# Kernel tuning notes

Hardware: AMD Instinct MI355X
Metric: run time of the kernel (lower is better)

## Reference

```python
import jax, jax.numpy as jnp
import numpy as np

LN_EPS = 1e-5


def _pos_embed_2d(w, h, c, dtype=jnp.float32):
    # matches build_2d_sincos_position_embedding: meshgrid indexing='xy' -> (h, w) grids
    grid_w = jnp.arange(w, dtype=jnp.float32)
    grid_h = jnp.arange(h, dtype=jnp.float32)
    gw, gh = jnp.meshgrid(grid_w, grid_h, indexing='xy')  # each (h, w)
    pos_dim = c // 4
    omega = 1.0 / (10000.0 ** (jnp.arange(pos_dim, dtype=jnp.float32) / pos_dim))
    out_w = gw.reshape(-1, 1) * omega[None]  # (h*w, pos_dim)
    out_h = gh.reshape(-1, 1) * omega[None]
    pe = jnp.concatenate([jnp.sin(out_w), jnp.cos(out_w), jnp.sin(out_h), jnp.cos(out_h)], axis=1)
    return pe.astype(dtype)  # (h*w, c)


def setup_inputs() -> dict:
    key = jax.random.key(0)
    k1, k2 = jax.random.split(key)
    N, C, H, W = 16, 256, 40, 40
    x = jax.random.normal(k1, (N, C, H, W), dtype=jnp.float32)
    ln_w = jnp.ones((C,), dtype=jnp.float32)
    ln_b = jnp.zeros((C,), dtype=jnp.float32)
    qkv_w = jax.random.normal(k2, (3 * C, C), dtype=jnp.float32) * 0.02  # 1x1 conv weight
    qkv_b = jnp.zeros((3 * C,), dtype=jnp.float32)
    gamma = jnp.ones((1,), dtype=jnp.float32)
    return {"x": x, "ln_w": ln_w, "ln_b": ln_b, "qkv_w": qkv_w, "qkv_b": qkv_b, "gamma": gamma}


def reference(x, ln_w, ln_b, qkv_w, qkv_b, gamma):
    N, C, H, W = x.shape
    scale = C ** (-0.5)
    identity = x

    # LayerNorm over channels (computed in NHWC like the torch permute dance)
    xh = jnp.transpose(x, (0, 2, 3, 1))  # (N, H, W, C)
    mu = jnp.mean(xh, axis=-1, keepdims=True)
    var = jnp.mean(jnp.square(xh - mu), axis=-1, keepdims=True)
    xn = (xh - mu) * jax.lax.rsqrt(var + LN_EPS) * ln_w + ln_b

    # 1x1 conv == per-pixel linear
    qkv = jnp.einsum('nhwc,oc->nhwo', xn, qkv_w) + qkv_b  # (N, H, W, 3C)
    qkv = qkv.reshape(N, H * W, 3 * C)
    q, k, v = jnp.split(qkv, 3, axis=-1)  # each (N, HW, C)

    pe = _pos_embed_2d(W, H, C, x.dtype)  # (HW, C)
    q = q + pe
    k = k + pe

    attn = jax.nn.softmax(jnp.einsum('nqc,nkc->nqk', q, k) * scale, axis=-1)
    out = jnp.einsum('nqk,nkc->nqc', attn, v)  # (N, HW, C)
    out = jnp.transpose(out, (0, 2, 1)).reshape(N, C, H, W)
    return identity + gamma[0] * out
```

## Files before the change

kernel.cpp:

```cpp
#include <hip/hip_runtime.h>
#include <hip/hip_bf16.h>

typedef float f32x4 __attribute__((ext_vector_type(4)));
typedef float f32x16 __attribute__((ext_vector_type(16)));
typedef __bf16 v8bf __attribute__((ext_vector_type(8)));
typedef unsigned short ushortx4 __attribute__((ext_vector_type(4)));
typedef unsigned short ushortx8 __attribute__((ext_vector_type(8)));
typedef unsigned int uint4v __attribute__((ext_vector_type(4)));

#define NIMG 16
#define CCH  256
#define HWP  1600

#define QSCALE 0.09016844f
#define DEFER_THR 2.885390f

__device__ __forceinline__ unsigned short f2bf(float f) {
  unsigned int u = __builtin_bit_cast(unsigned int, f);
  u = (u + 0x7FFFu + ((u >> 16) & 1u)) >> 16;
  return (unsigned short)u;
}

__device__ __forceinline__ f32x4 mfma16(v8bf a, v8bf b, f32x4 c) {
  return __builtin_amdgcn_mfma_f32_16x16x32_bf16(a, b, c, 0, 0, 0);
}

__device__ __forceinline__ unsigned cvtpk(float a, float b) {
  unsigned r;
  asm("v_cvt_pk_bf16_f32 %0, %1, %2" : "=v"(r) : "v"(a), "v"(b));
  return r;
}
__device__ __forceinline__ float exp2v(float x) {
  float r;
  asm("v_exp_f32 %0, %1" : "=v"(r) : "v"(x));
  return r;
}
__device__ __forceinline__ float sin2pi(float rev) {
  float r;
  asm("v_fract_f32 %0, %1\n\tv_sin_f32 %0, %0" : "=v"(r) : "v"(rev));
  return r;
}
#define PSWAP(a, b) asm("v_permlane32_swap_b32 %0, %1" : "+v"(a), "+v"(b))

__global__ void prep_kernel(const float* __restrict__ qkv_w,
                            float* __restrict__ pe,
                            unsigned short* __restrict__ w_frag) {
  int tid = blockIdx.x * blockDim.x + threadIdx.x;
  int nthr = gridDim.x * blockDim.x;
  for (int i = tid; i < 768 * 256; i += nthr) {
    int o = i >> 8, c = i & 255;
    int tile = o >> 4, lr = o & 15;
    int ks = c >> 5, lg = (c >> 3) & 3, e = c & 7;
    w_frag[(((size_t)tile * 8 + ks) * 64 + lg * 16 + lr) * 8 + e] = f2bf(qkv_w[i]);
  }
  const float oc = 0.20762051f;
  const float inv2pi = 0.15915494f;
  for (int i = tid; i < HWP * 256; i += nthr) {
    int p = i >> 8, c = i & 255;
    int j = p % 40, ii = p / 40;
    int tt = c & 63;
    float omega = exp2v(-(float)tt * oc) * inv2pi;
    float coord = (c < 128) ? (float)j : (float)ii;
    float rev = coord * omega;
    if (c & 64) rev += 0.25f;
    pe[i] = sin2pi(rev);
  }
}

__global__ __launch_bounds__(512, 4) void ln_qkv_kernel(
    const float* __restrict__ x, const float* __restrict__ ln_w, const float* __restrict__ ln_b,
    const unsigned short* __restrict__ w_frag, const float* __restrict__ qkv_b,
    const float* __restrict__ pe,
    unsigned short* __restrict__ q_arr, unsigned short* __restrict__ k_arr,
    unsigned short* __restrict__ v_arr) {
  __shared__ unsigned short bufraw[18432];
  __shared__ float red_s[8][64], red_q[8][64];
  __shared__ float mu_s[64], rs_s[64];

  int t = threadIdx.x;
  int n = blockIdx.x / 25, pt = blockIdx.x % 25;
  int pix0 = pt * 64;
  int p = t & 63, g = t >> 6;
  const float* xb = x + (size_t)n * CCH * HWP + pix0;

  {
    float sum = 0.f, sq = 0.f;
#pragma unroll
    for (int i = 0; i < 32; ++i) {
      float v = xb[(size_t)(g * 32 + i) * HWP + p];
      sum += v; sq += v * v;
    }
    red_s[g][p] = sum; red_q[g][p] = sq;
  }
  __syncthreads();
  if (t < 64) {
    float s = 0.f, q2 = 0.f;
#pragma unroll
    for (int gg = 0; gg < 8; ++gg) { s += red_s[gg][t]; q2 += red_q[gg][t]; }
    float mu = s * (1.f / 256.f);
    float var = q2 * (1.f / 256.f) - mu * mu;
    mu_s[t] = mu;
    rs_s[t] = rsqrtf(var + 1e-5f);
  }
  __syncthreads();
  {
    float mu = mu_s[p], rs = rs_s[p];
    int p7 = p & 7;
#pragma unroll
    for (int i4 = 0; i4 < 8; ++i4) {
      int c0 = g * 32 + i4 * 4;
      f32x4 lw = *(const f32x4*)&ln_w[c0];
      f32x4 lb = *(const f32x4*)&ln_b[c0];
      ushortx4 pk;
#pragma unroll
      for (int r = 0; r < 4; ++r) {
        float v = xb[(size_t)(c0 + r) * HWP + p];
        pk[r] = f2bf((v - mu) * rs * lw[r] + lb[r]);
      }
      int unit = (c0 >> 3) ^ p7;
      *(ushortx4*)&bufraw[p * 256 + unit * 8 + (i4 & 1) * 4] = pk;
    }
  }
  __syncthreads();

  int w = t >> 6, l = t & 63, lr = l & 15, lg = l >> 4;
  int lr7 = lr & 7;
  f32x4 acc[6][4];
#pragma unroll
  for (int nf = 0; nf < 6; ++nf)
#pragma unroll
    for (int mi = 0; mi < 4; ++mi) acc[nf][mi] = (f32x4){0.f, 0.f, 0.f, 0.f};

#pragma unroll
  for (int ks = 0; ks < 8; ++ks) {
    v8bf bF[4];
#pragma unroll
    for (int mi = 0; mi < 4; ++mi)
      bF[mi] = *(const v8bf*)&bufraw[(mi * 16 + lr) * 256 + (((ks * 4 + lg) ^ lr7) * 8)];
#pragma unroll
    for (int nf = 0; nf < 6; ++nf) {
      int tile = w + nf * 8;
      v8bf wf = *(const v8bf*)&w_frag[(((size_t)tile * 8 + ks) * 64 + l) * 8];
#pragma unroll
      for (int mi = 0; mi < 4; ++mi) acc[nf][mi] = mfma16(wf, bF[mi], acc[nf][mi]);
    }
  }
  __syncthreads();

  int lgh = lg >> 1, lgl = lg & 1;

#pragma unroll
  for (int nf = 4; nf < 6; ++nf) {
    int tile = w + nf * 8;
    f32x4 bi = *(const f32x4*)&qkv_b[tile * 16 + lg * 4];
    int chb = (nf - 4) * 16 + lg * 4;
#pragma unroll
    for (int mi = 0; mi < 4; ++mi) {
      int pixl = mi * 16 + lr;
      f32x4 vv = acc[nf][mi] + bi;
#pragma unroll
      for (int r = 0; r < 4; ++r)
        bufraw[(w * 32 + chb + r) * 72 + pixl] = f2bf(vv[r]);
    }
  }

#pragma unroll
  for (int nf = 0; nf < 2; ++nf) {
    int tile = w + nf * 8;
    f32x4 bi = *(const f32x4*)&qkv_b[tile * 16 + lg * 4];
#pragma unroll
    for (int mi = 0; mi < 4; ++mi) {
      int pix = pix0 + mi * 16 + lr;
      f32x4 pev = *(const f32x4*)&pe[(size_t)pix * 256 + tile * 16 + lg * 4];
      f32x4 vv = (acc[nf][mi] + bi + pev) * QSCALE;
      ushortx4 pk = {f2bf(vv[0]), f2bf(vv[1]), f2bf(vv[2]), f2bf(vv[3])};
      int qt = pix >> 5, l31 = pix & 31;
      size_t ad = ((((size_t)n * 50 + qt) * 16 + tile) * 2 + lgh) * 256 + l31 * 8 + lgl * 4;
      *(ushortx4*)&q_arr[ad] = pk;
    }
  }
#pragma unroll
  for (int nf = 2; nf < 4; ++nf) {
    int tile = w + nf * 8;
    int dt = tile - 16;
    f32x4 bi = *(const f32x4*)&qkv_b[tile * 16 + lg * 4];
#pragma unroll
    for (int mi = 0; mi < 4; ++mi) {
      int pix = pix0 + mi * 16 + lr;
      f32x4 pev = *(const f32x4*)&pe[(size_t)pix * 256 + dt * 16 + lg * 4];
      f32x4 vv = acc[nf][mi] + bi + pev;
      ushortx4 pk = {f2bf(vv[0]), f2bf(vv[1]), f2bf(vv[2]), f2bf(vv[3])};
      size_t ad = (((size_t)n * 16 + dt) * 1600 + pix) * 16 + lgh * 8 + lgl * 4;
      *(ushortx4*)&k_arr[ad] = pk;
    }
  }

#pragma unroll
  for (int c = 0; c < 4; ++c) {
    int ch = l & 31;
    int pg = (l >> 5) + c * 2;
    ushortx8 vv = *(const ushortx8*)&bufraw[(w * 32 + ch) * 72 + pg * 8];
    int kvsl = pg >> 1, hi2 = pg & 1;
    int d = (ch & 15) + w * 16 + (ch >> 4) * 128;
    size_t di = (((size_t)n * 100 + pt * 4 + kvsl) * 2 + hi2) * 256 + d;
    *(ushortx8*)&v_arr[di * 8] = vv;
  }
}

__global__ __launch_bounds__(128, 2) void attn_kernel(
    const unsigned short* __restrict__ q_arr, const unsigned short* __restrict__ k_arr,
    const unsigned short* __restrict__ v_arr, const float* __restrict__ x,
    const float* __restrict__ gamma, float* __restrict__ out) {
  __shared__ float sx[4][2][4][64][4];

  int t = threadIdx.x;
  int wv = t >> 6, l = t & 63;
  int l31 = l & 31, hi = l >> 5;
  int dto = wv * 8;
  int dto32 = wv * 4;
  int slot = blockIdx.x & 7, j = blockIdx.x >> 3;
  int n = slot + 8 * (j / 50);
  int qt = j % 50;
  int q0 = qt * 32;

  v8bf qf[8];
  {
    const unsigned short* qp = q_arr + (((size_t)n * 50 + qt) * 32 + hi) * 256 + l31 * 8;
#pragma unroll
    for (int i = 0; i < 8; ++i)
      qf[i] = *(const v8bf*)(qp + (dto + i) * 512);
  }

  f32x16 acc[4];
#pragma unroll
  for (int dd = 0; dd < 4; ++dd)
#pragma unroll
    for (int r = 0; r < 16; ++r) acc[dd][r] = 0.f;

  float m_run = -1e30f, l_run = 0.f;

  const unsigned short* kbase = k_arr + (size_t)n * (16 * 1600 * 16) +
                                (size_t)dto * 25600 + hi * 8;
  const unsigned short* vbase = v_arr + (size_t)n * (100 * 2 * 256 * 8) +
                                hi * 2048 + l31 * 8 + dto32 * 256;

  v8bf kc[8];
#pragma unroll
  for (int i = 0; i < 8; ++i)
    kc[i] = *(const v8bf*)(kbase + (size_t)i * 25600 + l31 * 16);

  f32x16 sA, sB;
#pragma unroll
  for (int r = 0; r < 16; ++r) sA[r] = 0.f;
#pragma unroll
  for (int i = 0; i < 8; ++i)
    sA = __builtin_amdgcn_mfma_f32_32x32x16_bf16(kc[i], qf[i], sA, 0, 0, 0);

#pragma unroll
  for (int r4 = 0; r4 < 4; ++r4) {
    f32x4 vv = {sA[r4 * 4 + 0], sA[r4 * 4 + 1], sA[r4 * 4 + 2], sA[r4 * 4 + 3]};
    *(f32x4*)&sx[0][wv][r4][l][0] = vv;
  }
#pragma unroll
  for (int i = 0; i < 8; ++i)
    kc[i] = *(const v8bf*)(kbase + (size_t)i * 25600 + (32 + l31) * 16);

  v8bf vf0[4], vf1[4];
#pragma unroll
  for (int i = 0; i < 4; ++i) vf0[i] = *(const v8bf*)(vbase + i * 256);
#pragma unroll
  for (int i = 0; i < 4; ++i) vf1[i] = *(const v8bf*)(vbase + 4096 + i * 256);

  auto body = [&](int kt, f32x16& scur, f32x16& snxt, bool nexttile) {
    asm volatile("s_waitcnt lgkmcnt(0)" ::: "memory");
    __builtin_amdgcn_s_barrier();
    int br = kt & 3;
    float p[16];
#pragma unroll
    for (int r4 = 0; r4 < 4; ++r4) {
      f32x4 oth = *(const f32x4*)&sx[br][wv ^ 1][r4][l][0];
#pragma unroll
      for (int rr = 0; rr < 4; ++rr)
        p[r4 * 4 + rr] = scur[r4 * 4 + rr] + oth[rr];
    }
    if (nexttile) {
#pragma unroll
      for (int r = 0; r < 16; ++r) snxt[r] = 0.f;
#pragma unroll
      for (int i = 0; i < 4; ++i)
        snxt = __builtin_amdgcn_mfma_f32_32x32x16_bf16(kc[i], qf[i], snxt, 0, 0, 0);
    }
    float t0 = fmaxf(p[0], p[1]), t1 = fmaxf(p[2], p[3]);
    float t2 = fmaxf(p[4], p[5]), t3 = fmaxf(p[6], p[7]);
    float t4 = fmaxf(p[8], p[9]), t5 = fmaxf(p[10], p[11]);
    float t6 = fmaxf(p[12], p[13]), t7 = fmaxf(p[14], p[15]);
    float mx = fmaxf(fmaxf(fmaxf(t0, t1), fmaxf(t2, t3)),
                     fmaxf(fmaxf(t4, t5), fmaxf(t6, t7)));
    mx = fmaxf(mx, __shfl_xor(mx, 32));
    if (!__all(mx <= m_run + DEFER_THR)) {
      float mnew = fmaxf(m_run, mx);
      float alpha = exp2v(m_run - mnew);
      l_run *= alpha;
#pragma unroll
      for (int dd = 0; dd < 4; ++dd)
#pragma unroll
        for (int r = 0; r < 16; ++r) acc[dd][r] *= alpha;
      m_run = mnew;
    }
    if (nexttile) {
#pragma unroll
      for (int i = 4; i < 8; ++i)
        snxt = __builtin_amdgcn_mfma_f32_32x32x16_bf16(kc[i], qf[i], snxt, 0, 0, 0);
    }
#pragma unroll
    for (int r = 0; r < 16; ++r) p[r] = exp2v(p[r] - m_run);
    float sSum = ((p[0] + p[1]) + (p[2] + p[3])) + ((p[4] + p[5]) + (p[6] + p[7])) +
                 (((p[8] + p[9]) + (p[10] + p[11])) + ((p[12] + p[13]) + (p[14] + p[15])));
    sSum += __shfl_xor(sSum, 32);
    l_run += sSum;

    unsigned x0 = cvtpk(p[0], p[1]), x1 = cvtpk(p[2], p[3]);
    unsigned y0 = cvtpk(p[4], p[5]), y1 = cvtpk(p[6], p[7]);
    PSWAP(x0, y0); PSWAP(x1, y1);
    uint4v u0 = {x0, x1, y0, y1};
    v8bf pf0 = __builtin_bit_cast(v8bf, u0);
    unsigned z0 = cvtpk(p[8], p[9]), z1 = cvtpk(p[10], p[11]);
    unsigned w0 = cvtpk(p[12], p[13]), w1 = cvtpk(p[14], p[15]);
    PSWAP(z0, w0); PSWAP(z1, w1);
    uint4v u1 = {z0, z1, w0, w1};
    v8bf pf1 = __builtin_bit_cast(v8bf, u1);

#pragma unroll
    for (int dd = 0; dd < 4; ++dd) {
      acc[dd] = __builtin_amdgcn_mfma_f32_32x32x16_bf16(vf0[dd], pf0, acc[dd], 0, 0, 0);
      acc[dd] = __builtin_amdgcn_mfma_f32_32x32x16_bf16(vf1[dd], pf1, acc[dd], 0, 0, 0);
    }

    if (nexttile) {
      int bw = (kt + 1) & 3;
#pragma unroll
      for (int r4 = 0; r4 < 4; ++r4) {
        f32x4 vv = {snxt[r4 * 4 + 0], snxt[r4 * 4 + 1], snxt[r4 * 4 + 2], snxt[r4 * 4 + 3]};
        *(f32x4*)&sx[bw][wv][r4][l][0] = vv;
      }
      int kt2 = (kt + 2 < 50) ? kt + 2 : 0;
#pragma unroll
      for (int i = 0; i < 8; ++i)
        kc[i] = *(const v8bf*)(kbase + (size_t)i * 25600 + (kt2 * 32 + l31) * 16);
      const unsigned short* vp = vbase + (size_t)(kt + 1) * 8192;
#pragma unroll
      for (int i = 0; i < 4; ++i) vf0[i] = *(const v8bf*)(vp + i * 256);
#pragma unroll
      for (int i = 0; i < 4; ++i) vf1[i] = *(const v8bf*)(vp + 4096 + i * 256);
    }
  };

  for (int kt = 0; kt < 48; kt += 2) {
    body(kt, sA, sB, true);
    body(kt + 1, sB, sA, true);
  }
  body(48, sA, sB, true);
  body(49, sB, sA, false);

  float inv = 1.f / l_run;
  float gm = gamma[0];
#pragma unroll
  for (int dd = 0; dd < 4; ++dd) {
#pragma unroll
    for (int r = 0; r < 16; ++r) {
      int d = (dto32 + dd) * 32 + (r & 3) + 8 * (r >> 2) + 4 * hi;
      size_t base = ((size_t)n * 256 + d) * HWP + q0 + l31;
      out[base] = x[base] + gm * acc[dd][r] * inv;
    }
  }
}

extern "C" void kernel_launch(void* const* d_in, const int* in_sizes, int n_in,
                              void* d_out, int out_size, void* d_ws, size_t ws_size,
                              hipStream_t stream) {
  const float* x     = (const float*)d_in[0];
  const float* ln_w  = (const float*)d_in[1];
  const float* ln_b  = (const float*)d_in[2];
  const float* qkv_w = (const float*)d_in[3];
  const float* qkv_b = (const float*)d_in[4];
  const float* gamma = (const float*)d_in[5];
  float* out = (float*)d_out;

  char* ws = (char*)d_ws;
  unsigned short* w_frag = (unsigned short*)ws;
  float*          pe     = (float*)(ws + 393216);
  unsigned short* q_arr  = (unsigned short*)(ws + 2031616);
  unsigned short* k_arr  = (unsigned short*)(ws + 15138816);
  unsigned short* v_arr  = (unsigned short*)(ws + 28246016);

  hipLaunchKernelGGL(prep_kernel, dim3(1024), dim3(256), 0, stream, qkv_w, pe, w_frag);
  hipLaunchKernelGGL(ln_qkv_kernel, dim3(400), dim3(512), 0, stream,
                     x, ln_w, ln_b, w_frag, qkv_b, pe, q_arr, k_arr, v_arr);
  hipLaunchKernelGGL(attn_kernel, dim3(800), dim3(128), 0, stream,
                     q_arr, k_arr, v_arr, x, gamma, out);
}
```

Before: 118.7 us.

## Warp-specialize attention into QK producer and softmax-PV consumer waves

```diff
diff --git a/kernel.cpp b/kernel.cpp
--- a/kernel.cpp
+++ b/kernel.cpp
@@ -20,9 +20,15 @@
   u = (u + 0x7FFFu + ((u >> 16) & 1u)) >> 16;
   return (unsigned short)u;
 }
+__device__ __forceinline__ float bf2f(unsigned short u) {
+  return __builtin_bit_cast(float, (unsigned int)u << 16);
+}
 
 __device__ __forceinline__ f32x4 mfma16(v8bf a, v8bf b, f32x4 c) {
   return __builtin_amdgcn_mfma_f32_16x16x32_bf16(a, b, c, 0, 0, 0);
+}
+__device__ __forceinline__ f32x16 mfma32(v8bf a, v8bf b, f32x16 c) {
+  return __builtin_amdgcn_mfma_f32_32x32x16_bf16(a, b, c, 0, 0, 0);
 }
 
 __device__ __forceinline__ unsigned cvtpk(float a, float b) {
@@ -43,7 +49,7 @@
 #define PSWAP(a, b) asm("v_permlane32_swap_b32 %0, %1" : "+v"(a), "+v"(b))
 
 __global__ void prep_kernel(const float* __restrict__ qkv_w,
-                            float* __restrict__ pe,
+                            unsigned short* __restrict__ pe16,
                             unsigned short* __restrict__ w_frag) {
   int tid = blockIdx.x * blockDim.x + threadIdx.x;
   int nthr = gridDim.x * blockDim.x;
@@ -63,14 +69,14 @@
     float coord = (c < 128) ? (float)j : (float)ii;
     float rev = coord * omega;
     if (c & 64) rev += 0.25f;
-    pe[i] = sin2pi(rev);
+    pe16[i] = f2bf(sin2pi(rev));
   }
 }
 
 __global__ __launch_bounds__(512, 4) void ln_qkv_kernel(
     const float* __restrict__ x, const float* __restrict__ ln_w, const float* __restrict__ ln_b,
     const unsigned short* __restrict__ w_frag, const float* __restrict__ qkv_b,
-    const float* __restrict__ pe,
+    const unsigned short* __restrict__ pe16,
     unsigned short* __restrict__ q_arr, unsigned short* __restrict__ k_arr,
     unsigned short* __restrict__ v_arr) {
   __shared__ unsigned short bufraw[18432];
@@ -83,12 +89,13 @@
   int p = t & 63, g = t >> 6;
   const float* xb = x + (size_t)n * CCH * HWP + pix0;
 
+  float xv[32];
   {
     float sum = 0.f, sq = 0.f;
 #pragma unroll
     for (int i = 0; i < 32; ++i) {
       float v = xb[(size_t)(g * 32 + i) * HWP + p];
-      sum += v; sq += v * v;
+      xv[i] = v; sum += v; sq += v * v;
     }
     red_s[g][p] = sum; red_q[g][p] = sq;
   }
@@ -113,10 +120,8 @@
       f32x4 lb = *(const f32x4*)&ln_b[c0];
       ushortx4 pk;
 #pragma unroll
-      for (int r = 0; r < 4; ++r) {
-        float v = xb[(size_t)(c0 + r) * HWP + p];
-        pk[r] = f2bf((v - mu) * rs * lw[r] + lb[r]);
-      }
+      for (int r = 0; r < 4; ++r)
+        pk[r] = f2bf((xv[i4 * 4 + r] - mu) * rs * lw[r] + lb[r]);
       int unit = (c0 >> 3) ^ p7;
       *(ushortx4*)&bufraw[p * 256 + unit * 8 + (i4 & 1) * 4] = pk;
     }
@@ -167,31 +172,23 @@
 #pragma unroll
   for (int nf = 0; nf < 2; ++nf) {
     int tile = w + nf * 8;
-    f32x4 bi = *(const f32x4*)&qkv_b[tile * 16 + lg * 4];
+    int c4 = tile * 16 + lg * 4;
+    f32x4 biq = *(const f32x4*)&qkv_b[c4];
+    f32x4 bik = *(const f32x4*)&qkv_b[256 + c4];
 #pragma unroll
     for (int mi = 0; mi < 4; ++mi) {
       int pix = pix0 + mi * 16 + lr;
-      f32x4 pev = *(const f32x4*)&pe[(size_t)pix * 256 + tile * 16 + lg * 4];
-      f32x4 vv = (acc[nf][mi] + bi + pev) * QSCALE;
-      ushortx4 pk = {f2bf(vv[0]), f2bf(vv[1]), f2bf(vv[2]), f2bf(vv[3])};
+      ushortx4 pu = *(const ushortx4*)&pe16[(size_t)pix * 256 + c4];
+      f32x4 pev = {bf2f(pu[0]), bf2f(pu[1]), bf2f(pu[2]), bf2f(pu[3])};
+      f32x4 vq = (acc[nf][mi] + biq + pev) * QSCALE;
+      ushortx4 pkq = {f2bf(vq[0]), f2bf(vq[1]), f2bf(vq[2]), f2bf(vq[3])};
       int qt = pix >> 5, l31 = pix & 31;
-      size_t ad = ((((size_t)n * 50 + qt) * 16 + tile) * 2 + lgh) * 256 + l31 * 8 + lgl * 4;
-      *(ushortx4*)&q_arr[ad] = pk;
-    }
-  }
-#pragma unroll
-  for (int nf = 2; nf < 4; ++nf) {
-    int tile = w + nf * 8;
-    int dt = tile - 16;
-    f32x4 bi = *(const f32x4*)&qkv_b[tile * 16 + lg * 4];
-#pragma unroll
-    for (int mi = 0; mi < 4; ++mi) {
-      int pix = pix0 + mi * 16 + lr;
-      f32x4 pev = *(const f32x4*)&pe[(size_t)pix * 256 + dt * 16 + lg * 4];
-      f32x4 vv = acc[nf][mi] + bi + pev;
-      ushortx4 pk = {f2bf(vv[0]), f2bf(vv[1]), f2bf(vv[2]), f2bf(vv[3])};
-      size_t ad = (((size_t)n * 16 + dt) * 1600 + pix) * 16 + lgh * 8 + lgl * 4;
-      *(ushortx4*)&k_arr[ad] = pk;
+      size_t adq = ((((size_t)n * 50 + qt) * 16 + tile) * 2 + lgh) * 256 + l31 * 8 + lgl * 4;
+      *(ushortx4*)&q_arr[adq] = pkq;
+      f32x4 vk = acc[nf + 2][mi] + bik + pev;
+      ushortx4 pkk = {f2bf(vk[0]), f2bf(vk[1]), f2bf(vk[2]), f2bf(vk[3])};
+      size_t adk = (((size_t)n * 16 + tile) * 1600 + pix) * 16 + lgh * 8 + lgl * 4;
+      *(ushortx4*)&k_arr[adk] = pkk;
     }
   }
 
@@ -207,170 +204,169 @@
   }
 }
 
-__global__ __launch_bounds__(128, 2) void attn_kernel(
+__global__ __launch_bounds__(256) void attn_kernel(
     const unsigned short* __restrict__ q_arr, const unsigned short* __restrict__ k_arr,
     const unsigned short* __restrict__ v_arr, const float* __restrict__ x,
     const float* __restrict__ gamma, float* __restrict__ out) {
-  __shared__ float sx[4][2][4][64][4];
+  __shared__ float sx[4][4][64][4];
 
   int t = threadIdx.x;
   int wv = t >> 6, l = t & 63;
   int l31 = l & 31, hi = l >> 5;
-  int dto = wv * 8;
-  int dto32 = wv * 4;
   int slot = blockIdx.x & 7, j = blockIdx.x >> 3;
   int n = slot + 8 * (j / 50);
   int qt = j % 50;
   int q0 = qt * 32;
 
-  v8bf qf[8];
-  {
-    const unsigned short* qp = q_arr + (((size_t)n * 50 + qt) * 32 + hi) * 256 + l31 * 8;
-#pragma unroll
-    for (int i = 0; i < 8; ++i)
-      qf[i] = *(const v8bf*)(qp + (dto + i) * 512);
-  }
-
-  f32x16 acc[4];
-#pragma unroll
-  for (int dd = 0; dd < 4; ++dd)
-#pragma unroll
-    for (int r = 0; r < 16; ++r) acc[dd][r] = 0.f;
-
-  float m_run = -1e30f, l_run = 0.f;
-
-  const unsigned short* kbase = k_arr + (size_t)n * (16 * 1600 * 16) +
-                                (size_t)dto * 25600 + hi * 8;
-  const unsigned short* vbase = v_arr + (size_t)n * (100 * 2 * 256 * 8) +
-                                hi * 2048 + l31 * 8 + dto32 * 256;
-
-  v8bf kc[8];
-#pragma unroll
-  for (int i = 0; i < 8; ++i)
-    kc[i] = *(const v8bf*)(kbase + (size_t)i * 25600 + l31 * 16);
-
-  f32x16 sA, sB;
-#pragma unroll
-  for (int r = 0; r < 16; ++r) sA[r] = 0.f;
-#pragma unroll
-  for (int i = 0; i < 8; ++i)
-    sA = __builtin_amdgcn_mfma_f32_32x32x16_bf16(kc[i], qf[i], sA, 0, 0, 0);
-
-#pragma unroll
-  for (int r4 = 0; r4 < 4; ++r4) {
-    f32x4 vv = {sA[r4 * 4 + 0], sA[r4 * 4 + 1], sA[r4 * 4 + 2], sA[r4 * 4 + 3]};
-    *(f32x4*)&sx[0][wv][r4][l][0] = vv;
-  }
-#pragma unroll
-  for (int i = 0; i < 8; ++i)
-    kc[i] = *(const v8bf*)(kbase + (size_t)i * 25600 + (32 + l31) * 16);
-
-  v8bf vf0[4], vf1[4];
-#pragma unroll
-  for (int i = 0; i < 4; ++i) vf0[i] = *(const v8bf*)(vbase + i * 256);
-#pragma unroll
-  for (int i = 0; i < 4; ++i) vf1[i] = *(const v8bf*)(vbase + 4096 + i * 256);
-
-  auto body = [&](int kt, f32x16& scur, f32x16& snxt, bool nexttile) {
-    asm volatile("s_waitcnt lgkmcnt(0)" ::: "memory");
-    __builtin_amdgcn_s_barrier();
-    int br = kt & 3;
-    float p[16];
+  if (wv < 2) {
+    int pw = wv;
+    v8bf qf[16];
+    {
+      const unsigned short* qp = q_arr + (((size_t)n * 50 + qt) * 32 + hi) * 256 + l31 * 8;
+#pragma unroll
+      for (int i = 0; i < 16; ++i) qf[i] = *(const v8bf*)(qp + i * 512);
+    }
+    const unsigned short* kbase = k_arr + (size_t)n * (16 * 1600 * 16) + hi * 8;
+
+    v8bf kc[16];
+#pragma unroll
+    for (int i = 0; i < 16; ++i)
+      kc[i] = *(const v8bf*)(kbase + (size_t)i * 25600 + (pw * 32 + l31) * 16);
+
+    f32x16 s0, s1;
+#pragma unroll
+    for (int r = 0; r < 16; ++r) { s0[r] = 0.f; s1[r] = 0.f; }
+#pragma unroll
+    for (int i = 0; i < 16; i += 2) {
+      s0 = mfma32(kc[i], qf[i], s0);
+      s1 = mfma32(kc[i + 1], qf[i + 1], s1);
+    }
 #pragma unroll
     for (int r4 = 0; r4 < 4; ++r4) {
-      f32x4 oth = *(const f32x4*)&sx[br][wv ^ 1][r4][l][0];
-#pragma unroll
-      for (int rr = 0; rr < 4; ++rr)
-        p[r4 * 4 + rr] = scur[r4 * 4 + rr] + oth[rr];
-    }
-    if (nexttile) {
-#pragma unroll
-      for (int r = 0; r < 16; ++r) snxt[r] = 0.f;
-#pragma unroll
-      for (int i = 0; i < 4; ++i)
-        snxt = __builtin_amdgcn_mfma_f32_32x32x16_bf16(kc[i], qf[i], snxt, 0, 0, 0);
-    }
-    float t0 = fmaxf(p[0], p[1]), t1 = fmaxf(p[2], p[3]);
-    float t2 = fmaxf(p[4], p[5]), t3 = fmaxf(p[6], p[7]);
-    float t4 = fmaxf(p[8], p[9]), t5 = fmaxf(p[10], p[11]);
-    float t6 = fmaxf(p[12], p[13]), t7 = fmaxf(p[14], p[15]);
-    float mx = fmaxf(fmaxf(fmaxf(t0, t1), fmaxf(t2, t3)),
-                     fmaxf(fmaxf(t4, t5), fmaxf(t6, t7)));
-    mx = fmaxf(mx, __shfl_xor(mx, 32));
-    if (!__all(mx <= m_run + DEFER_THR)) {
-      float mnew = fmaxf(m_run, mx);
-      float alpha = exp2v(m_run - mnew);
-      l_run *= alpha;
-#pragma unroll
-      for (int dd = 0; dd < 4; ++dd)
-#pragma unroll
-        for (int r = 0; r < 16; ++r) acc[dd][r] *= alpha;
-      m_run = mnew;
-    }
-    if (nexttile) {
-#pragma unroll
-      for (int i = 4; i < 8; ++i)
-        snxt = __builtin_amdgcn_mfma_f32_32x32x16_bf16(kc[i], qf[i], snxt, 0, 0, 0);
-    }
-#pragma unroll
-    for (int r = 0; r < 16; ++r) p[r] = exp2v(p[r] - m_run);
-    float sSum = ((p[0] + p[1]) + (p[2] + p[3])) + ((p[4] + p[5]) + (p[6] + p[7])) +
-                 (((p[8] + p[9]) + (p[10] + p[11])) + ((p[12] + p[13]) + (p[14] + p[15])));
-    sSum += __shfl_xor(sSum, 32);
-    l_run += sSum;
-
-    unsigned x0 = cvtpk(p[0], p[1]), x1 = cvtpk(p[2], p[3]);
-    unsigned y0 = cvtpk(p[4], p[5]), y1 = cvtpk(p[6], p[7]);
-    PSWAP(x0, y0); PSWAP(x1, y1);
-    uint4v u0 = {x0, x1, y0, y1};
-    v8bf pf0 = __builtin_bit_cast(v8bf, u0);
-    unsigned z0 = cvtpk(p[8], p[9]), z1 = cvtpk(p[10], p[11]);
-    unsigned w0 = cvtpk(p[12], p[13]), w1 = cvtpk(p[14], p[15]);
-    PSWAP(z0, w0); PSWAP(z1, w1);
-    uint4v u1 = {z0, z1, w0, w1};
-    v8bf pf1 = __builtin_bit_cast(v8bf, u1);
-
+      f32x4 vv = {s0[r4 * 4 + 0] + s1[r4 * 4 + 0], s0[r4 * 4 + 1] + s1[r4 * 4 + 1],
+                  s0[r4 * 4 + 2] + s1[r4 * 4 + 2], s0[r4 * 4 + 3] + s1[r4 * 4 + 3]};
+      *(f32x4*)&sx[pw][r4][l][0] = vv;
+    }
+#pragma unroll
+    for (int i = 0; i < 16; ++i)
+      kc[i] = *(const v8bf*)(kbase + (size_t)i * 25600 + ((pw + 2) * 32 + l31) * 16);
+
+    for (int it = 0; it < 50; ++it) {
+      asm volatile("s_waitcnt lgkmcnt(0)" ::: "memory");
+      __builtin_amdgcn_s_barrier();
+      if (((it & 1) == pw) && (it + 2 < 50)) {
+        int tt = it + 2;
+#pragma unroll
+        for (int r = 0; r < 16; ++r) { s0[r] = 0.f; s1[r] = 0.f; }
+#pragma unroll
+        for (int i = 0; i < 16; i += 2) {
+          s0 = mfma32(kc[i], qf[i], s0);
+          s1 = mfma32(kc[i + 1], qf[i + 1], s1);
+        }
+#pragma unroll
+        for (int r4 = 0; r4 < 4; ++r4) {
+          f32x4 vv = {s0[r4 * 4 + 0] + s1[r4 * 4 + 0], s0[r4 * 4 + 1] + s1[r4 * 4 + 1],
+                      s0[r4 * 4 + 2] + s1[r4 * 4 + 2], s0[r4 * 4 + 3] + s1[r4 * 4 + 3]};
+          *(f32x4*)&sx[tt & 3][r4][l][0] = vv;
+        }
+        int nt = (tt + 2 < 50) ? tt + 2 : 0;
+#pragma unroll
+        for (int i = 0; i < 16; ++i)
+          kc[i] = *(const v8bf*)(kbase + (size_t)i * 25600 + (nt * 32 + l31) * 16);
+      }
+    }
+  } else {
+    __builtin_amdgcn_s_setprio(1);
+    int dh = wv - 2;
+    int dto32 = dh * 4;
+    f32x16 acc[4];
+#pragma unroll
+    for (int dd = 0; dd < 4; ++dd)
+#pragma unroll
+      for (int r = 0; r < 16; ++r) acc[dd][r] = 0.f;
+    float m_run = -1e30f, l_run = 0.f;
+
+    const unsigned short* vbase = v_arr + (size_t)n * (100 * 2 * 256 * 8) +
+                                  hi * 2048 + l31 * 8 + dto32 * 256;
+    v8bf vA0[4], vA1[4], vB0[4], vB1[4];
+#pragma unroll
+    for (int i = 0; i < 4; ++i) vA0[i] = *(const v8bf*)(vbase + i * 256);
+#pragma unroll
+    for (int i = 0; i < 4; ++i) vA1[i] = *(const v8bf*)(vbase + 4096 + i * 256);
+
+    auto citer = [&](int it, v8bf (&c0)[4], v8bf (&c1)[4], v8bf (&n0)[4], v8bf (&n1)[4]) {
+      asm volatile("s_waitcnt lgkmcnt(0)" ::: "memory");
+      __builtin_amdgcn_s_barrier();
+      float p[16];
+#pragma unroll
+      for (int r4 = 0; r4 < 4; ++r4) {
+        f32x4 a = *(const f32x4*)&sx[it & 3][r4][l][0];
+#pragma unroll
+        for (int rr = 0; rr < 4; ++rr) p[r4 * 4 + rr] = a[rr];
+      }
+      if (it + 1 < 50) {
+        const unsigned short* vp = vbase + (size_t)(it + 1) * 8192;
+#pragma unroll
+        for (int i = 0; i < 4; ++i) n0[i] = *(const v8bf*)(vp + i * 256);
+#pragma unroll
+        for (int i = 0; i < 4; ++i) n1[i] = *(const v8bf*)(vp + 4096 + i * 256);
+      }
+      float t0 = fmaxf(p[0], p[1]), t1 = fmaxf(p[2], p[3]);
+      float t2 = fmaxf(p[4], p[5]), t3 = fmaxf(p[6], p[7]);
+      float t4 = fmaxf(p[8], p[9]), t5 = fmaxf(p[10], p[11]);
+      float t6 = fmaxf(p[12], p[13]), t7 = fmaxf(p[14], p[15]);
+      float mx = fmaxf(fmaxf(fmaxf(t0, t1), fmaxf(t2, t3)),
+                       fmaxf(fmaxf(t4, t5), fmaxf(t6, t7)));
+      mx = fmaxf(mx, __shfl_xor(mx, 32));
+      if (!__all(mx <= m_run + DEFER_THR)) {
+        float mnew = fmaxf(m_run, mx);
+        float alpha = exp2v(m_run - mnew);
+        l_run *= alpha;
+#pragma unroll
+        for (int dd = 0; dd < 4; ++dd)
+#pragma unroll
+          for (int r = 0; r < 16; ++r) acc[dd][r] *= alpha;
+        m_run = mnew;
+      }
+#pragma unroll
+      for (int r = 0; r < 16; ++r) p[r] = exp2v(p[r] - m_run);
+      float sSum = ((p[0] + p[1]) + (p[2] + p[3])) + ((p[4] + p[5]) + (p[6] + p[7])) +
+                   (((p[8] + p[9]) + (p[10] + p[11])) + ((p[12] + p[13]) + (p[14] + p[15])));
+      sSum += __shfl_xor(sSum, 32);
+      l_run += sSum;
+
+      unsigned x0 = cvtpk(p[0], p[1]), x1 = cvtpk(p[2], p[3]);
+      unsigned y0 = cvtpk(p[4], p[5]), y1 = cvtpk(p[6], p[7]);
+      PSWAP(x0, y0); PSWAP(x1, y1);
+      uint4v u0 = {x0, x1, y0, y1};
+      v8bf pf0 = __builtin_bit_cast(v8bf, u0);
+      unsigned z0 = cvtpk(p[8], p[9]), z1 = cvtpk(p[10], p[11]);
+      unsigned w0 = cvtpk(p[12], p[13]), w1 = cvtpk(p[14], p[15]);
+      PSWAP(z0, w0); PSWAP(z1, w1);
+      uint4v u1 = {z0, z1, w0, w1};
+      v8bf pf1 = __builtin_bit_cast(v8bf, u1);
+
+      acc[0] = mfma32(c0[0], pf0, acc[0]); acc[1] = mfma32(c0[1], pf0, acc[1]);
+      acc[2] = mfma32(c0[2], pf0, acc[2]); acc[3] = mfma32(c0[3], pf0, acc[3]);
+      acc[0] = mfma32(c1[0], pf1, acc[0]); acc[1] = mfma32(c1[1], pf1, acc[1]);
+      acc[2] = mfma32(c1[2], pf1, acc[2]); acc[3] = mfma32(c1[3], pf1, acc[3]);
+    };
+
+    for (int it = 0; it < 50; it += 2) {
+      citer(it, vA0, vA1, vB0, vB1);
+      citer(it + 1, vB0, vB1, vA0, vA1);
+    }
+
+    float inv = 1.f / l_run;
+    float gm = gamma[0];
 #pragma unroll
     for (int dd = 0; dd < 4; ++dd) {
-      acc[dd] = __builtin_amdgcn_mfma_f32_32x32x16_bf16(vf0[dd], pf0, acc[dd], 0, 0, 0);
-      acc[dd] = __builtin_amdgcn_mfma_f32_32x32x16_bf16(vf1[dd], pf1, acc[dd], 0, 0, 0);
-    }
-
-    if (nexttile) {
-      int bw = (kt + 1) & 3;
-#pragma unroll
-      for (int r4 = 0; r4 < 4; ++r4) {
-        f32x4 vv = {snxt[r4 * 4 + 0], snxt[r4 * 4 + 1], snxt[r4 * 4 + 2], snxt[r4 * 4 + 3]};
-        *(f32x4*)&sx[bw][wv][r4][l][0] = vv;
-      }
-      int kt2 = (kt + 2 < 50) ? kt + 2 : 0;
-#pragma unroll
-      for (int i = 0; i < 8; ++i)
-        kc[i] = *(const v8bf*)(kbase + (size_t)i * 25600 + (kt2 * 32 + l31) * 16);
-      const unsigned short* vp = vbase + (size_t)(kt + 1) * 8192;
-#pragma unroll
-      for (int i = 0; i < 4; ++i) vf0[i] = *(const v8bf*)(vp + i * 256);
-#pragma unroll
-      for (int i = 0; i < 4; ++i) vf1[i] = *(const v8bf*)(vp + 4096 + i * 256);
-    }
-  };
-
-  for (int kt = 0; kt < 48; kt += 2) {
-    body(kt, sA, sB, true);
-    body(kt + 1, sB, sA, true);
-  }
-  body(48, sA, sB, true);
-  body(49, sB, sA, false);
-
-  float inv = 1.f / l_run;
-  float gm = gamma[0];
-#pragma unroll
-  for (int dd = 0; dd < 4; ++dd) {
-#pragma unroll
-    for (int r = 0; r < 16; ++r) {
-      int d = (dto32 + dd) * 32 + (r & 3) + 8 * (r >> 2) + 4 * hi;
-      size_t base = ((size_t)n * 256 + d) * HWP + q0 + l31;
-      out[base] = x[base] + gm * acc[dd][r] * inv;
+#pragma unroll
+      for (int r = 0; r < 16; ++r) {
+        int d = (dto32 + dd) * 32 + (r & 3) + 8 * (r >> 2) + 4 * hi;
+        size_t base = ((size_t)n * 256 + d) * HWP + q0 + l31;
+        out[base] = x[base] + gm * acc[dd][r] * inv;
+      }
     }
   }
 }
@@ -388,14 +384,14 @@
 
   char* ws = (char*)d_ws;
   unsigned short* w_frag = (unsigned short*)ws;
-  float*          pe     = (float*)(ws + 393216);
+  unsigned short* pe16   = (unsigned short*)(ws + 393216);
   unsigned short* q_arr  = (unsigned short*)(ws + 2031616);
   unsigned short* k_arr  = (unsigned short*)(ws + 15138816);
   unsigned short* v_arr  = (unsigned short*)(ws + 28246016);
 
-  hipLaunchKernelGGL(prep_kernel, dim3(1024), dim3(256), 0, stream, qkv_w, pe, w_frag);
+  hipLaunchKernelGGL(prep_kernel, dim3(1024), dim3(256), 0, stream, qkv_w, pe16, w_frag);
   hipLaunchKernelGGL(ln_qkv_kernel, dim3(400), dim3(512), 0, stream,
-                     x, ln_w, ln_b, w_frag, qkv_b, pe, q_arr, k_arr, v_arr);
-  hipLaunchKernelGGL(attn_kernel, dim3(800), dim3(128), 0, stream,
+                     x, ln_w, ln_b, w_frag, qkv_b, pe16, q_arr, k_arr, v_arr);
+  hipLaunchKernelGGL(attn_kernel, dim3(800), dim3(256), 0, stream,
                      q_arr, k_arr, v_arr, x, gamma, out);
 }
```

Result: slower. 131.9 us (+11.1%).
